# Kernel tuning notes

Measured on AMD Instinct MI355X. Metric: run time of the kernel, lower is better.

## Reference

```python
import jax, jax.numpy as jnp
import numpy as np
from jax import lax

HIDDEN = 256
WIDTH = 1024
DEPTH = 4
T = 64
SUBSTEPS = 8  # fixed RK4 substeps per save interval (replaces diffrax adaptive Tsit5)

Y0 = np.array([0.0008417, 0.01495894, 0.00082556, 0.00068982, 0.00063456,
               0.00832867, 0.00190631, 0.00155624, 0.00142264, 0.01858621,
               0.02000239, 0.01796071, 0.01670121, 0.22218046, 0.02531468,
               0.03337227, 0.6147068], dtype=np.float32)


def setup_inputs() -> dict:
    key = jax.random.key(0)
    ks = jax.random.split(key, 8)

    def lin(k, out, inp):
        kw, kb = jax.random.split(k)
        lim = 1.0 / np.sqrt(inp)
        W = jax.random.uniform(kw, (out, inp), jnp.float32, -lim, lim)
        b = jax.random.uniform(kb, (out,), jnp.float32, -lim, lim)
        return W, b

    W0, b0 = lin(ks[0], WIDTH, HIDDEN + 17)
    Whs, bhs = [], []
    for i in range(DEPTH - 1):
        w, b = lin(ks[1 + i], WIDTH, WIDTH)
        Whs.append(w)
        bhs.append(b)
    Wh = jnp.stack(Whs)   # [DEPTH-1, WIDTH, WIDTH]
    bh = jnp.stack(bhs)   # [DEPTH-1, WIDTH]
    Wl, bl = lin(ks[4], HIDDEN, WIDTH)
    beta_W, beta_b = lin(ks[5], 1, HIDDEN)
    hvec = 0.01 * jax.random.normal(ks[6], (HIDDEN,), jnp.float32)
    scale = jnp.array([0.1], jnp.float32)
    y0_log = jnp.log(jnp.asarray(Y0))
    ts = jnp.arange(T, dtype=jnp.float32) * 0.25  # save points (months)
    return dict(ts=ts, W0=W0, b0=b0, Wh=Wh, bh=bh, Wl=Wl, bl=bl,
                beta_W=beta_W, beta_b=beta_b, hvec=hvec, scale=scale,
                y0_log=y0_log)


def _forward(ts, W0, b0, Wh, bh, Wl, bl, beta_W, beta_b, hvec, scale, y0_log):
    xi, mu, sigma, nu, gamma = 13/12, 0.041/12, 91/12, 36/12, 1.8/12

    def mlp(x):  # softplus hidden activations, final tanh(0.01*x)
        z = jax.nn.softplus(W0 @ x + b0)
        def body(z, wb):
            w, b = wb
            return jax.nn.softplus(w @ z + b), None
        z, _ = lax.scan(body, z, (Wh, bh))
        return jnp.tanh(0.01 * (Wl @ z + bl))

    def rhs(y):  # y = concat(state[17], h[HIDDEN])
        state, h = y[:17], y[17:]
        bb1 = 8.0 * jax.nn.sigmoid(beta_W @ h + beta_b)[0] + 25.0
        bb2, bb3, bb4 = 0.5 * bb1, 0.35 * bb1, 0.25 * bb1
        M, S1, E1, E2, E3, E4, I1, I2, I3, I4, R1, R2, R3, R4, S2, S3, S4 = state
        I = I1 + I2 + I3 + I4
        R = R1 + R2 + R3 + R4
        dstate = jnp.stack([
            R * mu - (xi + mu) * M,
            mu * (1 - R) + xi * M - mu * S1 - bb1 * I * S1,
            bb1 * I * S1 - (mu + sigma) * E1,
            bb2 * I * S2 - (mu + sigma) * E2,
            bb3 * I * S3 - (mu + sigma) * E3,
            bb4 * I * S4 - (mu + sigma) * E4,
            sigma * E1 - (nu + mu) * I1,
            sigma * E2 - (nu + mu) * I2,
            sigma * E3 - (nu + mu) * I3,
            sigma * E4 - (nu + mu) * I4,
            nu * I1 - (mu + gamma) * R1,
            nu * I2 - (mu + gamma) * R2,
            nu * I3 - (mu + gamma) * R3,
            nu * I4 - (mu + gamma) * R4,
            gamma * R1 - mu * S2 - bb2 * I * S2,
            gamma * R2 - mu * S3 - bb3 * I * S3,
            gamma * (R3 + R4) - mu * S4 - bb4 * I * S4,
        ])
        dh = scale[0] * mlp(jnp.concatenate([h, state]))
        return jnp.concatenate([dstate, dh])

    def rk4(y, dt):
        k1 = rhs(y)
        k2 = rhs(y + 0.5 * dt * k1)
        k3 = rhs(y + 0.5 * dt * k2)
        k4 = rhs(y + dt * k3)
        return y + (dt / 6.0) * (k1 + 2 * k2 + 2 * k3 + k4)

    y0 = jnp.concatenate([jax.nn.softmax(y0_log), hvec])

    def interval(y, dt_i):
        dt = dt_i / SUBSTEPS
        def step(y, _):
            return rk4(y, dt), None
        y, _ = lax.scan(step, y, None, length=SUBSTEPS)
        return y, y

    dts = ts[1:] - ts[:-1]
    _, ys = lax.scan(interval, y0, dts)
    ys = jnp.concatenate([y0[None], ys], axis=0)  # [T, 17+HIDDEN]
    return ys[:, :17], ys[:, 17:]


def reference(ts, W0, b0, Wh, bh, Wl, bl, beta_W, beta_b, hvec, scale, y0_log):
    return _forward(ts, W0, b0, Wh, bh, Wl, bl, beta_W, beta_b, hvec, scale, y0_log)
```

## Files before the change

kernel.cpp:

```cpp
#include <hip/hip_runtime.h>
#include <math.h>

#define NBLK    32
#define NLAUNCH 256
#define BS      512
#define NSTATE  17
#define NH      256
#define NX      273
#define WID     1024
#define NT      64
#define NSUB    8
#define ROWS_H  (WID/NBLK)
#define ROWS_L  (NH/NBLK)
#define POLL_CAP 2000000

typedef unsigned int u32;

__device__ __forceinline__ float softplus_f(float v) {
    return fmaxf(v, 0.f) + log1pf(expf(-fabsf(v)));
}

#define FLG_STRIDE 16

__device__ __forceinline__ void flag_add(u32* flags, unsigned R) {
    u32* fp = flags + (R & 7) * FLG_STRIDE;
    asm volatile("global_atomic_add %0, %1, off" :: "v"(fp), "v"(1u) : "memory");
}
__device__ __forceinline__ u32 flag_read(u32* flags, unsigned R) {
    u32* fp = flags + (R & 7) * FLG_STRIDE;
    u32 cur;
    asm volatile("global_atomic_add %0, %1, %2, off sc0\n\t"
                 "s_waitcnt vmcnt(0)"
                 : "=&v"(cur) : "v"(fp), "v"(0u) : "memory");
    return cur;
}
__device__ __forceinline__ void publish(u32* flags, unsigned R, int t) {
    asm volatile("s_waitcnt vmcnt(0)" ::: "memory");
    __syncthreads();
    if (t == 0) flag_add(flags, R);
}
__device__ __forceinline__ void wait_flag(u32* flags, unsigned R, int t) {
    if (t == 0) {
        const unsigned tgt = (unsigned)NBLK * (((R - 1) >> 3) + 1);
        int it = 0;
        while (flag_read(flags, R) < tgt && ++it < POLL_CAP) {}
    }
    __syncthreads();
    asm volatile("buffer_inv" ::: "memory");
}
__device__ __forceinline__ void consume_z(const float* __restrict__ buf,
                                          u32* flags, unsigned R,
                                          float* __restrict__ z_s, int t) {
    wait_flag(flags, R, t);
    float2 v = *(const float2*)(buf + 2 * t);
    *(float2*)(z_s + 2 * t) = v;
    __syncthreads();
}

extern "C" __global__ __launch_bounds__(BS, 2) void ode_kernel(
    const float* __restrict__ ts,   const float* __restrict__ W0,
    const float* __restrict__ b0,   const float* __restrict__ Wh,
    const float* __restrict__ bh,   const float* __restrict__ Wl,
    const float* __restrict__ bl,   const float* __restrict__ betaW,
    const float* __restrict__ betab,const float* __restrict__ hvec,
    const float* __restrict__ scale,const float* __restrict__ y0log,
    float* __restrict__ out, float* zA, float* zB, float* dhb,
    u32* flags, unsigned* ctrl)
{
    const int t = threadIdx.x;

    __shared__ int   role_sh;
    __shared__ float y_s[NX];
    __shared__ float yn_s[NX];
    __shared__ float xm[NX];
    __shared__ float k_s[NX];
    __shared__ float z_s[WID];
    __shared__ float red[8];
    __shared__ float dt_sh;
    extern __shared__ float wh2[];

    if (t == 0) {
        int xcd;
        asm volatile("s_getreg_b32 %0, hwreg(HW_REG_XCC_ID)" : "=s"(xcd));
        xcd &= 7;
        unsigned rk = atomicAdd(&ctrl[xcd], 1u);
        if (rk == NBLK - 1) atomicCAS(&ctrl[8], 0u, (unsigned)(xcd + 1));
        unsigned w; int it = 0;
        do {
            w = __hip_atomic_load(&ctrl[8], __ATOMIC_RELAXED, __HIP_MEMORY_SCOPE_AGENT);
        } while (w == 0u && ++it < POLL_CAP);
        role_sh = (w != 0u && xcd == (int)w - 1 && rk < NBLK) ? (int)rk : -1;
    }
    __syncthreads();
    const int blk = role_sh;
    if (blk < 0) return;

    const float scale0 = scale[0];
    const float betab0 = betab[0];
    unsigned R = 0;

    const int rowH = t >> 4, laneH = t & 15;
    const int growH = blk * ROWS_H + rowH;
    const int rowL = t >> 6, laneL = t & 63;
    const int growL = blk * ROWS_L + rowL;

    const float b0r = b0[growH];
    float bhr[3];
    bhr[0] = bh[growH]; bhr[1] = bh[WID + growH]; bhr[2] = bh[2 * WID + growH];
    const float blr    = bl[growL];
    const float betaWr = (t < NH) ? betaW[t] : 0.f;
    const float* wlp = Wl + (size_t)growL * WID + laneL * 4;

    float4 wv0[16], wv1[16];
    {
        const float* whp = Wh + (size_t)growH * WID + laneH * 4;
        #pragma unroll
        for (int i = 0; i < 16; i++) wv0[i] = *(const float4*)(whp + i * 64);
        #pragma unroll
        for (int i = 0; i < 16; i++) wv1[i] = *(const float4*)(whp + WID * WID + i * 64);
    }
    {
        const float* src = Wh + 2 * (size_t)WID * WID + (size_t)blk * ROWS_H * WID;
        for (int i = t * 4; i < ROWS_H * WID; i += BS * 4)
            *(float4*)&wh2[i] = *(const float4*)&src[i];
    }
    float w0r[18];
    {
        const float* w0p = W0 + (size_t)growH * NX;
        #pragma unroll
        for (int i = 0; i < 18; i++) {
            int c = laneH + i * 16;
            w0r[i] = (c < NX) ? w0p[c] : 0.f;
        }
    }

    if (t < NSTATE) {
        float m = -1e30f;
        for (int j = 0; j < NSTATE; j++) m = fmaxf(m, y0log[j]);
        float ssum = 0.f;
        for (int j = 0; j < NSTATE; j++) ssum += expf(y0log[j] - m);
        y_s[t] = expf(y0log[t] - m) / ssum;
    }
    if (t < NH) y_s[NSTATE + t] = hvec[t];
    __syncthreads();

    if (blk == 0) {
        if (t < NSTATE) out[t] = y_s[t];
        if (t < NH)     out[NT * NSTATE + t] = y_s[NSTATE + t];
    }

    const float c_xi = 13.f / 12.f, c_mu = 0.041f / 12.f, c_sig = 91.f / 12.f,
                c_nu = 36.f / 12.f, c_gam = 1.8f / 12.f;

    for (int iv = 0; iv < NT - 1; iv++) {
        if (t == 0) dt_sh = (ts[iv + 1] - ts[iv]) * (1.f / NSUB);
        __syncthreads();
        const float dt = dt_sh;

        for (int sub = 0; sub < NSUB; sub++) {
            if (t < NX) yn_s[t] = y_s[t];

            for (int s = 0; s < 4; s++) {
                const float a   = (s == 0) ? 0.f : ((s == 3) ? 1.f : 0.5f);
                const float wgt = ((s == 0) || (s == 3)) ? dt * (1.f / 6.f) : dt * (1.f / 3.f);
                const float adt = a * dt;

                if (t < NX) {
                    const int src = (t < NH) ? (NSTATE + t) : (t - NH);
                    float v = y_s[src];
                    if (s != 0) v = fmaf(adt, k_s[src], v);
                    xm[t] = v;
                }
                __syncthreads();

                {
                    float acc = 0.f;
                    #pragma unroll
                    for (int i = 0; i < 18; i++) {
                        int c = laneH + i * 16;
                        if (c < NX) acc = fmaf(w0r[i], xm[c], acc);
                    }
                    #pragma unroll
                    for (int m = 1; m < 16; m <<= 1) acc += __shfl_xor(acc, m, 16);
                    if (laneH == 0) zA[growH] = softplus_f(acc + b0r);
                    ++R;
                    publish(flags, R, t);
                }

                {
                    if (t < NH) {
                        float p = betaWr * xm[t];
                        #pragma unroll
                        for (int m = 1; m < 64; m <<= 1) p += __shfl_xor(p, m, 64);
                        if ((t & 63) == 0) red[t >> 6] = p;
                    }
                    __syncthreads();
                    if (t == 0) {
                        const float* xs = xm + NH;
                        float sd  = red[0] + red[1] + red[2] + red[3] + betab0;
                        float bb1 = 8.f / (1.f + expf(-sd)) + 25.f;
                        float bb2 = 0.5f * bb1, bb3 = 0.35f * bb1, bb4 = 0.25f * bb1;
                        float M  = xs[0],  S1 = xs[1],  E1 = xs[2],  E2 = xs[3];
                        float E3 = xs[4],  E4 = xs[5],  I1 = xs[6],  I2 = xs[7];
                        float I3 = xs[8],  I4 = xs[9],  R1 = xs[10], R2 = xs[11];
                        float R3 = xs[12], R4 = xs[13], S2 = xs[14], S3 = xs[15];
                        float S4 = xs[16];
                        float I = I1 + I2 + I3 + I4, Rs = R1 + R2 + R3 + R4;
                        k_s[0]  = Rs * c_mu - (c_xi + c_mu) * M;
                        k_s[1]  = c_mu * (1.f - Rs) + c_xi * M - c_mu * S1 - bb1 * I * S1;
                        k_s[2]  = bb1 * I * S1 - (c_mu + c_sig) * E1;
                        k_s[3]  = bb2 * I * S2 - (c_mu + c_sig) * E2;
                        k_s[4]  = bb3 * I * S3 - (c_mu + c_sig) * E3;
                        k_s[5]  = bb4 * I * S4 - (c_mu + c_sig) * E4;
                        k_s[6]  = c_sig * E1 - (c_nu + c_mu) * I1;
                        k_s[7]  = c_sig * E2 - (c_nu + c_mu) * I2;
                        k_s[8]  = c_sig * E3 - (c_nu + c_mu) * I3;
                        k_s[9]  = c_sig * E4 - (c_nu + c_mu) * I4;
                        k_s[10] = c_nu * I1 - (c_mu + c_gam) * R1;
                        k_s[11] = c_nu * I2 - (c_mu + c_gam) * R2;
                        k_s[12] = c_nu * I3 - (c_mu + c_gam) * R3;
                        k_s[13] = c_nu * I4 - (c_mu + c_gam) * R4;
                        k_s[14] = c_gam * R1 - c_mu * S2 - bb2 * I * S2;
                        k_s[15] = c_gam * R2 - c_mu * S3 - bb3 * I * S3;
                        k_s[16] = c_gam * (R3 + R4) - c_mu * S4 - bb4 * I * S4;
                    }
                }

                auto hidden = [&](const float4 (&wv)[16], const float* zin,
                                  float* zout, float bias) {
                    consume_z(zin, flags, R, z_s, t);
                    float acc = 0.f;
                    #pragma unroll
                    for (int i = 0; i < 16; i++) {
                        float4 zv = *(const float4*)(z_s + (laneH * 4 + i * 64));
                        acc = fmaf(wv[i].x, zv.x, acc);
                        acc = fmaf(wv[i].y, zv.y, acc);
                        acc = fmaf(wv[i].z, zv.z, acc);
                        acc = fmaf(wv[i].w, zv.w, acc);
                    }
                    #pragma unroll
                    for (int m = 1; m < 16; m <<= 1) acc += __shfl_xor(acc, m, 16);
                    if (laneH == 0) zout[growH] = softplus_f(acc + bias);
                    ++R;
                    publish(flags, R, t);
                };

                hidden(wv0, zA, zB, bhr[0]);
                hidden(wv1, zB, zA, bhr[1]);

                float4 wvL[4];
                #pragma unroll
                for (int i = 0; i < 4; i++) wvL[i] = *(const float4*)(wlp + i * 256);

                {
                    consume_z(zA, flags, R, z_s, t);
                    const float* wr = wh2 + rowH * WID + laneH * 4;
                    float acc = 0.f;
                    #pragma unroll
                    for (int i = 0; i < 16; i++) {
                        float4 wv4 = *(const float4*)(wr + i * 64);
                        float4 zv  = *(const float4*)(z_s + (laneH * 4 + i * 64));
                        acc = fmaf(wv4.x, zv.x, acc);
                        acc = fmaf(wv4.y, zv.y, acc);
                        acc = fmaf(wv4.z, zv.z, acc);
                        acc = fmaf(wv4.w, zv.w, acc);
                    }
                    #pragma unroll
                    for (int m = 1; m < 16; m <<= 1) acc += __shfl_xor(acc, m, 16);
                    if (laneH == 0) zB[growH] = softplus_f(acc + bhr[2]);
                    ++R;
                    publish(flags, R, t);
                }

                {
                    consume_z(zB, flags, R, z_s, t);
                    float acc = 0.f;
                    #pragma unroll
                    for (int i = 0; i < 4; i++) {
                        float4 zv = *(const float4*)(z_s + (laneL * 4 + i * 256));
                        acc = fmaf(wvL[i].x, zv.x, acc);
                        acc = fmaf(wvL[i].y, zv.y, acc);
                        acc = fmaf(wvL[i].z, zv.z, acc);
                        acc = fmaf(wvL[i].w, zv.w, acc);
                    }
                    #pragma unroll
                    for (int m = 1; m < 64; m <<= 1) acc += __shfl_xor(acc, m, 64);
                    if (laneL == 0) dhb[growL] = scale0 * tanhf(0.01f * (acc + blr));
                    ++R;
                    publish(flags, R, t);
                }

                {
                    wait_flag(flags, R, t);
                    if (t < NH) k_s[NSTATE + t] = dhb[t];
                    __syncthreads();
                    if (t < NX) yn_s[t] = fmaf(wgt, k_s[t], yn_s[t]);
                }
            }

            __syncthreads();
            if (t < NX) y_s[t] = yn_s[t];
            __syncthreads();
        }

        if (blk == 0) {
            if (t < NSTATE) out[(iv + 1) * NSTATE + t] = y_s[t];
            if (t < NH)     out[NT * NSTATE + (iv + 1) * NH + t] = y_s[NSTATE + t];
        }
    }
}

extern "C" void kernel_launch(void* const* d_in, const int* in_sizes, int n_in,
                              void* d_out, int out_size, void* d_ws, size_t ws_size,
                              hipStream_t stream) {
    const float* ts    = (const float*)d_in[0];
    const float* W0    = (const float*)d_in[1];
    const float* b0    = (const float*)d_in[2];
    const float* Wh    = (const float*)d_in[3];
    const float* bh    = (const float*)d_in[4];
    const float* Wl    = (const float*)d_in[5];
    const float* bl    = (const float*)d_in[6];
    const float* betaW = (const float*)d_in[7];
    const float* betab = (const float*)d_in[8];
    const float* hvec  = (const float*)d_in[9];
    const float* scale = (const float*)d_in[10];
    const float* y0log = (const float*)d_in[11];
    float* out = (float*)d_out;

    float*    zA    = (float*)d_ws;
    float*    zB    = (float*)((char*)d_ws + 4096);
    float*    dhb   = (float*)((char*)d_ws + 8192);
    u32*      flags = (u32*)((char*)d_ws + 9216);
    unsigned* ctrl  = (unsigned*)((char*)d_ws + 9728);

    static int lds_set = 0;
    if (!lds_set) {
        hipFuncSetAttribute((const void*)ode_kernel,
                            hipFuncAttributeMaxDynamicSharedMemorySize, 131072);
        lds_set = 1;
    }

    hipMemsetAsync(d_ws, 0, 10240, stream);
    hipLaunchKernelGGL(ode_kernel, dim3(NLAUNCH), dim3(BS), 131072, stream,
                       ts, W0, b0, Wh, bh, Wl, bl, betaW, betab, hvec, scale,
                       y0log, out, zA, zB, dhb, flags, ctrl);
}
```

Baseline: 22.30 ms.

## Replace shared counter barrier with per-block arrival flags and atomic payload exchange

```diff
diff --git a/kernel.cpp b/kernel.cpp
--- a/kernel.cpp
+++ b/kernel.cpp
@@ -14,46 +14,82 @@
 #define ROWS_L  (NH/NBLK)
 #define POLL_CAP 2000000
 
+typedef unsigned long long u64;
 typedef unsigned int u32;
 
 __device__ __forceinline__ float softplus_f(float v) {
     return fmaxf(v, 0.f) + log1pf(expf(-fabsf(v)));
 }
 
-#define FLG_STRIDE 16
-
-__device__ __forceinline__ void flag_add(u32* flags, unsigned R) {
-    u32* fp = flags + (R & 7) * FLG_STRIDE;
-    asm volatile("global_atomic_add %0, %1, off" :: "v"(fp), "v"(1u) : "memory");
-}
-__device__ __forceinline__ u32 flag_read(u32* flags, unsigned R) {
-    u32* fp = flags + (R & 7) * FLG_STRIDE;
-    u32 cur;
+#define ARR_STRIDE 16
+
+__device__ __forceinline__ void swap_x2(u64* p, u64 w) {
+    asm volatile("global_atomic_swap_x2 %0, %1, off" :: "v"(p), "v"(w) : "memory");
+}
+__device__ __forceinline__ u64 add0_x2(const u64* p) {
+    u64 w;
+    asm volatile("global_atomic_add_x2 %0, %1, %2, off sc0\n\t"
+                 "s_waitcnt vmcnt(0)"
+                 : "=&v"(w) : "v"(p), "v"(0ULL) : "memory");
+    return w;
+}
+__device__ __forceinline__ void arr_set(u32* arr, int blk, u32 Rv) {
+    u32* p = arr + blk * ARR_STRIDE;
+    asm volatile("global_atomic_swap %0, %1, off" :: "v"(p), "v"(Rv) : "memory");
+}
+__device__ __forceinline__ u32 arr_get(u32* arr, int idx) {
+    u32* p = arr + idx * ARR_STRIDE;
+    u32 v;
     asm volatile("global_atomic_add %0, %1, %2, off sc0\n\t"
                  "s_waitcnt vmcnt(0)"
-                 : "=&v"(cur) : "v"(fp), "v"(0u) : "memory");
-    return cur;
-}
-__device__ __forceinline__ void publish(u32* flags, unsigned R, int t) {
-    asm volatile("s_waitcnt vmcnt(0)" ::: "memory");
-    __syncthreads();
-    if (t == 0) flag_add(flags, R);
-}
-__device__ __forceinline__ void wait_flag(u32* flags, unsigned R, int t) {
-    if (t == 0) {
-        const unsigned tgt = (unsigned)NBLK * (((R - 1) >> 3) + 1);
+                 : "=&v"(v) : "v"(p), "v"(0u) : "memory");
+    return v;
+}
+
+__device__ __forceinline__ void publish32(u64* z64, u32* arr, unsigned R,
+                                          float* pair_s, int t, int blk,
+                                          int rowH, int laneH, float val) {
+    if (laneH == 0) pair_s[rowH] = val;
+    __syncthreads();
+    if (t < 16) {
+        u64 w = ((u64)__float_as_uint(pair_s[2 * t + 1]) << 32)
+              |  (u64)__float_as_uint(pair_s[2 * t]);
+        swap_x2(z64 + blk * 16 + t, w);
+    }
+    if (t < 64) asm volatile("s_waitcnt vmcnt(0)" ::: "memory");
+    if (t == 0) arr_set(arr, blk, R);
+}
+__device__ __forceinline__ void publish8(u64* dh64, u32* arr, unsigned R,
+                                         float* pair_s, int t, int blk,
+                                         int rowL, int laneL, float val) {
+    if (laneL == 0) pair_s[rowL] = val;
+    __syncthreads();
+    if (t < 4) {
+        u64 w = ((u64)__float_as_uint(pair_s[2 * t + 1]) << 32)
+              |  (u64)__float_as_uint(pair_s[2 * t]);
+        swap_x2(dh64 + blk * 4 + t, w);
+    }
+    if (t < 64) asm volatile("s_waitcnt vmcnt(0)" ::: "memory");
+    if (t == 0) arr_set(arr, blk, R);
+}
+__device__ __forceinline__ void wait_all(u32* arr, unsigned R, int t) {
+    if (t < 64) {
+        const int idx = t & 31;
         int it = 0;
-        while (flag_read(flags, R) < tgt && ++it < POLL_CAP) {}
-    }
-    __syncthreads();
-    asm volatile("buffer_inv" ::: "memory");
-}
-__device__ __forceinline__ void consume_z(const float* __restrict__ buf,
-                                          u32* flags, unsigned R,
-                                          float* __restrict__ z_s, int t) {
-    wait_flag(flags, R, t);
-    float2 v = *(const float2*)(buf + 2 * t);
-    *(float2*)(z_s + 2 * t) = v;
+        for (;;) {
+            u32 v = arr_get(arr, idx);
+            if (__all((int)(v >= R))) break;
+            if (++it > POLL_CAP) break;
+        }
+    }
+    __syncthreads();
+}
+__device__ __forceinline__ void consume_z(const u64* z64, u32* arr, unsigned R,
+                                          float* z_s, int t) {
+    wait_all(arr, R, t);
+    u64 w = add0_x2(z64 + t);
+    z_s[2 * t]     = __uint_as_float((u32)w);
+    z_s[2 * t + 1] = __uint_as_float((u32)(w >> 32));
     __syncthreads();
 }
 
@@ -64,8 +100,8 @@
     const float* __restrict__ bl,   const float* __restrict__ betaW,
     const float* __restrict__ betab,const float* __restrict__ hvec,
     const float* __restrict__ scale,const float* __restrict__ y0log,
-    float* __restrict__ out, float* zA, float* zB, float* dhb,
-    u32* flags, unsigned* ctrl)
+    float* __restrict__ out, u64* zA64, u64* zB64, u64* dh64,
+    u32* arr, unsigned* ctrl)
 {
     const int t = threadIdx.x;
 
@@ -76,6 +112,7 @@
     __shared__ float k_s[NX];
     __shared__ float z_s[WID];
     __shared__ float red[8];
+    __shared__ float pair_s[ROWS_H];
     __shared__ float dt_sh;
     extern __shared__ float wh2[];
 
@@ -182,9 +219,9 @@
                     }
                     #pragma unroll
                     for (int m = 1; m < 16; m <<= 1) acc += __shfl_xor(acc, m, 16);
-                    if (laneH == 0) zA[growH] = softplus_f(acc + b0r);
                     ++R;
-                    publish(flags, R, t);
+                    publish32(zA64, arr, R, pair_s, t, blk, rowH, laneH,
+                              softplus_f(acc + b0r));
                 }
 
                 {
@@ -226,9 +263,9 @@
                     }
                 }
 
-                auto hidden = [&](const float4 (&wv)[16], const float* zin,
-                                  float* zout, float bias) {
-                    consume_z(zin, flags, R, z_s, t);
+                auto hidden = [&](const float4 (&wv)[16], const u64* zin64,
+                                  u64* zout64, float bias) {
+                    consume_z(zin64, arr, R, z_s, t);
                     float acc = 0.f;
                     #pragma unroll
                     for (int i = 0; i < 16; i++) {
@@ -240,20 +277,20 @@
                     }
                     #pragma unroll
                     for (int m = 1; m < 16; m <<= 1) acc += __shfl_xor(acc, m, 16);
-                    if (laneH == 0) zout[growH] = softplus_f(acc + bias);
                     ++R;
-                    publish(flags, R, t);
+                    publish32(zout64, arr, R, pair_s, t, blk, rowH, laneH,
+                              softplus_f(acc + bias));
                 };
 
-                hidden(wv0, zA, zB, bhr[0]);
-                hidden(wv1, zB, zA, bhr[1]);
+                hidden(wv0, zA64, zB64, bhr[0]);
+                hidden(wv1, zB64, zA64, bhr[1]);
 
                 float4 wvL[4];
                 #pragma unroll
                 for (int i = 0; i < 4; i++) wvL[i] = *(const float4*)(wlp + i * 256);
 
                 {
-                    consume_z(zA, flags, R, z_s, t);
+                    consume_z(zA64, arr, R, z_s, t);
                     const float* wr = wh2 + rowH * WID + laneH * 4;
                     float acc = 0.f;
                     #pragma unroll
@@ -267,13 +304,13 @@
                     }
                     #pragma unroll
                     for (int m = 1; m < 16; m <<= 1) acc += __shfl_xor(acc, m, 16);
-                    if (laneH == 0) zB[growH] = softplus_f(acc + bhr[2]);
                     ++R;
-                    publish(flags, R, t);
-                }
-
-                {
-                    consume_z(zB, flags, R, z_s, t);
+                    publish32(zB64, arr, R, pair_s, t, blk, rowH, laneH,
+                              softplus_f(acc + bhr[2]));
+                }
+
+                {
+                    consume_z(zB64, arr, R, z_s, t);
                     float acc = 0.f;
                     #pragma unroll
                     for (int i = 0; i < 4; i++) {
@@ -285,14 +322,18 @@
                     }
                     #pragma unroll
                     for (int m = 1; m < 64; m <<= 1) acc += __shfl_xor(acc, m, 64);
-                    if (laneL == 0) dhb[growL] = scale0 * tanhf(0.01f * (acc + blr));
                     ++R;
-                    publish(flags, R, t);
-                }
-
-                {
-                    wait_flag(flags, R, t);
-                    if (t < NH) k_s[NSTATE + t] = dhb[t];
+                    publish8(dh64, arr, R, pair_s, t, blk, rowL, laneL,
+                             scale0 * tanhf(0.01f * (acc + blr)));
+                }
+
+                {
+                    wait_all(arr, R, t);
+                    if (t < 128) {
+                        u64 w = add0_x2(dh64 + t);
+                        k_s[NSTATE + 2 * t]     = __uint_as_float((u32)w);
+                        k_s[NSTATE + 2 * t + 1] = __uint_as_float((u32)(w >> 32));
+                    }
                     __syncthreads();
                     if (t < NX) yn_s[t] = fmaf(wgt, k_s[t], yn_s[t]);
                 }
@@ -327,11 +368,11 @@
     const float* y0log = (const float*)d_in[11];
     float* out = (float*)d_out;
 
-    float*    zA    = (float*)d_ws;
-    float*    zB    = (float*)((char*)d_ws + 4096);
-    float*    dhb   = (float*)((char*)d_ws + 8192);
-    u32*      flags = (u32*)((char*)d_ws + 9216);
-    unsigned* ctrl  = (unsigned*)((char*)d_ws + 9728);
+    u64*      zA64 = (u64*)d_ws;
+    u64*      zB64 = (u64*)((char*)d_ws + 4096);
+    u64*      dh64 = (u64*)((char*)d_ws + 8192);
+    u32*      arr  = (u32*)((char*)d_ws + 9216);
+    unsigned* ctrl = (unsigned*)((char*)d_ws + 11264);
 
     static int lds_set = 0;
     if (!lds_set) {
@@ -340,8 +381,8 @@
         lds_set = 1;
     }
 
-    hipMemsetAsync(d_ws, 0, 10240, stream);
+    hipMemsetAsync(d_ws, 0, 11328, stream);
     hipLaunchKernelGGL(ode_kernel, dim3(NLAUNCH), dim3(BS), 131072, stream,
                        ts, W0, b0, Wh, bh, Wl, bl, betaW, betab, hvec, scale,
-                       y0log, out, zA, zB, dhb, flags, ctrl);
-}
+                       y0log, out, zA64, zB64, dh64, arr, ctrl);
+}
```

After: 44.23 ms. +98.3%, slower.
